# Kernel optimization log

Measured on AMD Instinct MI355X. Metric: run time of the kernel, lower is better.

Reference implementation:

```python
import jax, jax.numpy as jnp
import numpy as np

N_NODES = 50000
N_EDGES = 800000
F_IN = 128
UNIQUE_USER = 64
HIDDEN = 64
HEADS = 4


def _glorot(key, shape):
    fan_in, fan_out = shape[0], shape[-1]
    lim = (6.0 / (fan_in + fan_out)) ** 0.5
    return jax.random.uniform(key, shape, jnp.float32, -lim, lim)


def setup_inputs() -> dict:
    key = jax.random.key(0)
    ks = jax.random.split(key, 16)
    x = jax.random.normal(ks[0], (N_NODES, F_IN), jnp.float32)
    edge_index = jax.random.randint(ks[1], (2, N_EDGES), 0, N_NODES, jnp.int64)
    return {
        "x": x,
        "edge_index": edge_index,
        # lazy Linear layers (PyG Linear: y = x @ W + b)
        "lin1_w": _glorot(ks[2], (F_IN, UNIQUE_USER)),
        "lin1_b": jnp.zeros((UNIQUE_USER,), jnp.float32),
        "lin2_w": _glorot(ks[3], (F_IN, HIDDEN)),
        "lin2_b": jnp.zeros((HIDDEN,), jnp.float32),
        "lin3_w": _glorot(ks[4], (HIDDEN, HIDDEN)),
        "lin3_b": jnp.zeros((HIDDEN,), jnp.float32),
        # FeaStConv 1: in=UNIQUE_USER, out=HIDDEN, heads=HEADS
        "conv1_w": _glorot(ks[5], (UNIQUE_USER, HEADS * HIDDEN)),
        "conv1_u": _glorot(ks[6], (UNIQUE_USER, HEADS)),
        "conv1_c": jnp.zeros((HEADS,), jnp.float32),
        "conv1_bias": jnp.zeros((HIDDEN,), jnp.float32),
        # FeaStConv 2: in=HIDDEN, out=HIDDEN, heads=HEADS
        "conv2_w": _glorot(ks[7], (HIDDEN, HEADS * HIDDEN)),
        "conv2_u": _glorot(ks[8], (HIDDEN, HEADS)),
        "conv2_c": jnp.zeros((HEADS,), jnp.float32),
        "conv2_bias": jnp.zeros((HIDDEN,), jnp.float32),
    }


def feast_conv(x, edge_index, w, u, c, bias):
    # PyG FeaStConv, add_self_loops=False, aggr='mean'
    src, dst = edge_index[0], edge_index[1]  # message flows src(j) -> dst(i)
    x_j = x[src]                              # [E, Fin] gather
    x_i = x[dst]                              # [E, Fin] gather
    heads = u.shape[1]
    out_ch = w.shape[1] // heads
    # attention over heads: q = softmax((x_j - x_i) @ u + c)
    q = jax.nn.softmax((x_j - x_i) @ u + c, axis=-1)          # [E, H]
    w3 = w.reshape(w.shape[0], heads, out_ch)                  # [Fin, H, D]
    # message_e = sum_h q[e,h] * (x_j[e] @ W_h)
    msg = jnp.einsum('ef,fhd,eh->ed', x_j, w3, q)              # [E, D]
    agg = jax.ops.segment_sum(msg, dst, num_segments=N_NODES)  # [N, D]
    cnt = jax.ops.segment_sum(jnp.ones((msg.shape[0],), msg.dtype), dst,
                              num_segments=N_NODES)
    out = agg / jnp.clip(cnt, 1.0)[:, None]
    return out + bias


def reference(x, edge_index, lin1_w, lin1_b, lin2_w, lin2_b, lin3_w, lin3_b,
              conv1_w, conv1_u, conv1_c, conv1_bias,
              conv2_w, conv2_u, conv2_c, conv2_bias):
    h = feast_conv(x @ lin1_w + lin1_b, edge_index,
                   conv1_w, conv1_u, conv1_c, conv1_bias) + (x @ lin2_w + lin2_b)
    h = jax.nn.relu(h)
    h = feast_conv(h, edge_index,
                   conv2_w, conv2_u, conv2_c, conv2_bias) + (h @ lin3_w + lin3_b)
    return jax.nn.relu(h)
```

## Files before the change

### kernel.cpp

```cpp
#include <hip/hip_runtime.h>

#define NN 50000
#define NE 800000
#define NBUCK ((NN + 255) / 256)
#define EPB 4096
#define BCAP 8192
#define QCAP 512

typedef unsigned int uint32;
typedef unsigned short ushort16;
typedef __attribute__((ext_vector_type(8))) short bf16x8;
typedef __attribute__((ext_vector_type(4))) float f32x4;

__device__ __forceinline__ ushort16 f2bf(float f) {
    uint32 u = __float_as_uint(f);
    u += 0x7fff + ((u >> 16) & 1);
    return (ushort16)(u >> 16);
}
__device__ __forceinline__ float bf_lo(uint32 u) {
    return __uint_as_float(u << 16);
}
__device__ __forceinline__ float bf_hi(uint32 u) {
    return __uint_as_float(u & 0xffff0000u);
}
__device__ __forceinline__ bf16x8 pack8(const float4 a, const float4 b) {
    union { bf16x8 v; ushort16 u[8]; } r;
    r.u[0] = f2bf(a.x); r.u[1] = f2bf(a.y); r.u[2] = f2bf(a.z); r.u[3] = f2bf(a.w);
    r.u[4] = f2bf(b.x); r.u[5] = f2bf(b.y); r.u[6] = f2bf(b.z); r.u[7] = f2bf(b.w);
    return r.v;
}
__device__ __forceinline__ float4 softq(const float4 ts, const float4 td,
                                        const float4 tc, const float invdeg) {
    const float l0 = ts.x - td.x + tc.x;
    const float l1 = ts.y - td.y + tc.y;
    const float l2 = ts.z - td.z + tc.z;
    const float l3 = ts.w - td.w + tc.w;
    const float mx = fmaxf(fmaxf(l0, l1), fmaxf(l2, l3));
    const float e0 = __expf(l0 - mx);
    const float e1 = __expf(l1 - mx);
    const float e2 = __expf(l2 - mx);
    const float e3 = __expf(l3 - mx);
    const float sden = invdeg / (e0 + e1 + e2 + e3);
    return make_float4(e0 * sden, e1 * sden, e2 * sden, e3 * sden);
}

__device__ __forceinline__ float multireduce16(const float* tl, int m) {
    float t8[8];
#pragma unroll
    for (int i = 0; i < 8; ++i) {
        const float a0 = tl[2 * i], b0 = tl[2 * i + 1];
        const float oa = __shfl_xor(a0, 1, 64), ob = __shfl_xor(b0, 1, 64);
        t8[i] = ((m & 1) == 0) ? (a0 + oa) : (b0 + ob);
    }
    float t4[4];
#pragma unroll
    for (int i = 0; i < 4; ++i) {
        const float a0 = t8[2 * i], b0 = t8[2 * i + 1];
        const float oa = __shfl_xor(a0, 2, 64), ob = __shfl_xor(b0, 2, 64);
        t4[i] = ((m & 2) == 0) ? (a0 + oa) : (b0 + ob);
    }
    float t2[2];
#pragma unroll
    for (int i = 0; i < 2; ++i) {
        const float a0 = t4[2 * i], b0 = t4[2 * i + 1];
        const float oa = __shfl_xor(a0, 4, 64), ob = __shfl_xor(b0, 4, 64);
        t2[i] = ((m & 4) == 0) ? (a0 + oa) : (b0 + ob);
    }
    const float a0 = t2[0], b0 = t2[1];
    const float oa = __shfl_xor(a0, 8, 64), ob = __shfl_xor(b0, 8, 64);
    return ((m & 8) == 0) ? (a0 + oa) : (b0 + ob);
}

__device__ __forceinline__ ushort16 packp_val(const float* __restrict__ w, int i) {
    const int j  = i & 7;
    const int ln = (i >> 3) & 63;
    const int s  = (i >> 9) & 7;
    const int cc = i >> 12;
    const int k  = s * 32 + ((ln >> 4) * 8) + j;
    const int n  = cc * 16 + (ln & 15);
    return f2bf(w[(k >> 2) * 256 + (k & 3) * 64 + n]);
}

__global__ __launch_bounds__(256) void k_packall(
    const float* __restrict__ w1, const float* __restrict__ w2,
    const float* __restrict__ wc1, const float* __restrict__ wc2,
    const float* __restrict__ wl3,
    ushort16* __restrict__ pw12, ushort16* __restrict__ pwc1,
    ushort16* __restrict__ pwc2, ushort16* __restrict__ pwl3,
    int* __restrict__ bcnt)
{
    const int gid = blockIdx.x * 256 + threadIdx.x;
    if (gid < 16384) {
        const int i = gid;
        const int j  = i & 7;
        const int ln = (i >> 3) & 63;
        const int s  = (i >> 9) & 3;
        const int cc = i >> 11;
        const int k  = s * 32 + ((ln >> 4) * 8) + j;
        const int n  = cc * 16 + (ln & 15);
        pw12[i] = f2bf((n < 64) ? w1[k * 64 + n] : w2[k * 64 + (n - 64)]);
    } else if (gid < 32768) {
        pwc1[gid - 16384] = packp_val(wc1, gid - 16384);
    } else if (gid < 49152) {
        pwc2[gid - 32768] = packp_val(wc2, gid - 32768);
    } else if (gid < 53248) {
        const int i = gid - 49152;
        const int j  = i & 7;
        const int ln = (i >> 3) & 63;
        const int s  = (i >> 9) & 1;
        const int cc = i >> 10;
        const int k  = s * 32 + ((ln >> 4) * 8) + j;
        const int n  = cc * 16 + (ln & 15);
        pwl3[i] = f2bf(wl3[k * 64 + n]);
    } else if (gid < 53504) {
        bcnt[gid - 53248] = 0;
    }
}

__global__ __launch_bounds__(256) void k_lin12(
    const float* __restrict__ x, const ushort16* __restrict__ pw,
    const float* __restrict__ b1, const float* __restrict__ b2,
    const float* __restrict__ u,
    ushort16* __restrict__ ab, float* __restrict__ skip,
    float* __restrict__ tOut)
{
    const int tid = threadIdx.x;
    const int lane = tid & 63;
    const int g = tid >> 6;
    const int m = lane & 15;
    const int quad = lane >> 4;
    const int rowBase = blockIdx.x * 64 + g * 16;

    const int arow = min(rowBase + m, NN - 1);
    const float* xr = x + (size_t)arow * 128 + quad * 8;

    f32x4 acc[8];
#pragma unroll
    for (int c = 0; c < 8; ++c)
#pragma unroll
        for (int r = 0; r < 4; ++r) acc[c][r] = 0.f;

#pragma unroll
    for (int s = 0; s < 4; ++s) {
        const float4 xa = *(const float4*)(xr + s * 32);
        const float4 xb = *(const float4*)(xr + s * 32 + 4);
        const bf16x8 af = pack8(xa, xb);
#pragma unroll
        for (int c = 0; c < 8; ++c) {
            const bf16x8 bf = *(const bf16x8*)&pw[((c * 4 + s) * 64 + lane) * 8];
            acc[c] = __builtin_amdgcn_mfma_f32_16x16x32_bf16(af, bf, acc[c], 0, 0, 0);
        }
    }

    float tl[16];
#pragma unroll
    for (int i = 0; i < 16; ++i) tl[i] = 0.f;

#pragma unroll
    for (int c = 0; c < 8; ++c) {
        const int colg = c * 16 + m;
        const float bv = (colg < 64) ? b1[colg] : b2[colg - 64];
#pragma unroll
        for (int reg = 0; reg < 4; ++reg) {
            const float v = acc[c][reg] + bv;
            const int gr = rowBase + quad * 4 + reg;
            if (gr < NN) {
                if (c < 4) ab[gr * 64 + colg] = f2bf(v);
                else       skip[gr * 64 + (colg - 64)] = v;
            }
            if (c < 4) {
                const float4 uv = ((const float4*)u)[colg];
                tl[reg * 4 + 0] += v * uv.x;
                tl[reg * 4 + 1] += v * uv.y;
                tl[reg * 4 + 2] += v * uv.z;
                tl[reg * 4 + 3] += v * uv.w;
            }
        }
    }

    const float tv = multireduce16(tl, m);
    const int gidx = rowBase * 4 + (quad << 4) + m;
    if (gidx < NN * 4) tOut[gidx] = tv;
}

__global__ __launch_bounds__(256) void k_lin3m(
    const ushort16* __restrict__ hb, const ushort16* __restrict__ pw,
    const float* __restrict__ b, float* __restrict__ outp)
{
    const int tid = threadIdx.x;
    const int lane = tid & 63;
    const int g = tid >> 6;
    const int m = lane & 15;
    const int quad = lane >> 4;
    const int rowBase = blockIdx.x * 64 + g * 16;

    const int arow = min(rowBase + m, NN - 1);
    const ushort16* zrow = hb + (size_t)arow * 64 + quad * 8;

    f32x4 acc[4];
#pragma unroll
    for (int c = 0; c < 4; ++c)
#pragma unroll
        for (int r = 0; r < 4; ++r) acc[c][r] = 0.f;

#pragma unroll
    for (int s = 0; s < 2; ++s) {
        const bf16x8 af = *(const bf16x8*)(zrow + s * 32);
#pragma unroll
        for (int c = 0; c < 4; ++c) {
            const bf16x8 bf = *(const bf16x8*)&pw[((c * 2 + s) * 64 + lane) * 8];
            acc[c] = __builtin_amdgcn_mfma_f32_16x16x32_bf16(af, bf, acc[c], 0, 0, 0);
        }
    }

#pragma unroll
    for (int c = 0; c < 4; ++c) {
        const int colg = c * 16 + m;
        const float bv = b[colg];
#pragma unroll
        for (int reg = 0; reg < 4; ++reg) {
            const int gr = rowBase + quad * 4 + reg;
            if (gr < NN) outp[gr * 64 + colg] = acc[c][reg] + bv;
        }
    }
}

__global__ __launch_bounds__(256) void k_bin(const int* __restrict__ ei,
                                             int* __restrict__ bcnt,
                                             uint32* __restrict__ pairs)
{
    __shared__ int hist[NBUCK];
    __shared__ int gbase[NBUCK];
    const int t = threadIdx.x;
    const int base = blockIdx.x * EPB;

    for (int b = t; b < NBUCK; b += 256) hist[b] = 0;
    __syncthreads();

    uint32 pk[16];
    int bk[16], rk[16];
#pragma unroll
    for (int k = 0; k < 16; ++k) {
        const int e = base + k * 256 + t;
        if (e < NE) {
            const int s = ei[e];
            const int d = ei[NE + e];
            bk[k] = d >> 8;
            pk[k] = (uint32)s | ((uint32)(d & 255) << 16);
            rk[k] = atomicAdd(&hist[bk[k]], 1);
        }
    }
    __syncthreads();

    for (int b = t; b < NBUCK; b += 256)
        gbase[b] = hist[b] ? atomicAdd(&bcnt[b], hist[b]) : 0;
    __syncthreads();

#pragma unroll
    for (int k = 0; k < 16; ++k) {
        const int e = base + k * 256 + t;
        if (e < NE) pairs[(size_t)bk[k] * BCAP + gbase[bk[k]] + rk[k]] = pk[k];
    }
}

__global__ __launch_bounds__(256) void k_binscat(const uint32* __restrict__ pairs,
                                                 const int* __restrict__ bcnt,
                                                 int* __restrict__ row_ptr,
                                                 int* __restrict__ ssrc)
{
    __shared__ int sb[256];
    __shared__ int hist[256];
    __shared__ int s[256];
    __shared__ int lptr[256];
    __shared__ int lcur[256];
    const int b = blockIdx.x;
    const int t = threadIdx.x;
    const int total = bcnt[b];
    const uint32* pb = pairs + (size_t)b * BCAP;

    sb[t] = (t < NBUCK) ? bcnt[t] : 0;
    __syncthreads();
    for (int off = 1; off < 256; off <<= 1) {
        const int v = (t >= off) ? sb[t - off] : 0;
        __syncthreads();
        sb[t] += v;
        __syncthreads();
    }
    const int base = sb[b] - total;
    if (b == 0 && t == 0) row_ptr[NN] = NE;

    hist[t] = 0;
    __syncthreads();
    for (int e = t; e < total; e += 256) atomicAdd(&hist[pb[e] >> 16], 1);
    __syncthreads();

    const int v = hist[t];
    s[t] = v;
    __syncthreads();
    for (int off = 1; off < 256; off <<= 1) {
        const int u = (t >= off) ? s[t - off] : 0;
        __syncthreads();
        s[t] += u;
        __syncthreads();
    }
    const int excl = base + s[t] - v;
    lptr[t] = excl;
    lcur[t] = 0;
    const int n = (b << 8) + t;
    if (n < NN) row_ptr[n] = excl;
    __syncthreads();

    for (int e = t; e < total; e += 256) {
        const uint32 p = pb[e];
        const int d = p >> 16;
        const int r = atomicAdd(&lcur[d], 1);
        ssrc[lptr[d] + r] = (int)(p & 0xffffu);
    }
}

__global__ __launch_bounds__(256) void k_aggpost(
    const int* __restrict__ row_ptr, const int* __restrict__ ssrc,
    const float* __restrict__ t, const uint32* __restrict__ abu,
    const float* __restrict__ c,
    const ushort16* __restrict__ pw, const float* __restrict__ bias,
    const float* __restrict__ skip,
    float* __restrict__ out, ushort16* __restrict__ outb,
    const float* __restrict__ uproj, float* __restrict__ tOut)
{
    __shared__ float4 ql[QCAP];
    __shared__ char zl[16 * 512];
    __shared__ float t_lds[4][64];
    __shared__ float4 tnode[16];
    __shared__ float invdegs[16];

    const int tid = threadIdx.x;
    const int lane = tid & 63;
    const int w = tid >> 6;
    const int half = lane >> 5;
    const int u = lane & 31;
    const int nodeBase = blockIdx.x * 16;

    const float4 tc = *(const float4*)c;

    int rr = 0;
    if (lane < 7) {
        const int off = (lane < 5) ? (w * 4 + lane) : ((lane == 5) ? 0 : 16);
        rr = row_ptr[nodeBase + off];
    }
    const int rp0 = __shfl(rr, 0, 64);
    const int rp1 = __shfl(rr, 1, 64);
    const int rp2 = __shfl(rr, 2, 64);
    const int rp3 = __shfl(rr, 3, 64);
    const int rp4 = __shfl(rr, 4, 64);
    const int r0b = __shfl(rr, 5, 64);
    const int r1b = __shfl(rr, 6, 64);

    if (lane < 4) {
        tnode[w * 4 + lane] = ((const float4*)t)[nodeBase + w * 4 + lane];
        const int a = (lane == 0) ? rp0 : (lane == 1) ? rp1 : (lane == 2) ? rp2 : rp3;
        const int b = (lane == 0) ? rp1 : (lane == 1) ? rp2 : (lane == 2) ? rp3 : rp4;
        invdegs[w * 4 + lane] = (b > a) ? 1.f / (float)(b - a) : 0.f;
    }

    const bool fit = (r1b - r0b) <= QCAP;

    if (fit) {
        for (int i = rp0 + lane; i < rp4; i += 64) {
            const int se = ssrc[i];
            const int dl = (i >= rp1) + (i >= rp2) + (i >= rp3);
            const float4 ts = ((const float4*)t)[se];
            const float4 q = softq(ts, tnode[w * 4 + dl], tc, invdegs[w * 4 + dl]);
            ql[i - r0b] = make_float4(q.y, q.z, q.w, __int_as_float(se));
        }
    }

#define ACCUM3(QA, AV)                                                 \
    {                                                                  \
        const float v0 = bf_lo(AV), v1 = bf_hi(AV);                    \
        const float q0 = invdeg - (QA).x - (QA).y - (QA).z;            \
        z00 += q0 * v0;     z01 += q0 * v1;                            \
        z10 += (QA).x * v0; z11 += (QA).x * v1;                        \
        z20 += (QA).y * v0; z21 += (QA).y * v1;                        \
        z30 += (QA).z * v0; z31 += (QA).z * v1;                        \
    }
#define ACCUM4(Q4, AV)                                                 \
    {                                                                  \
        const float v0 = bf_lo(AV), v1 = bf_hi(AV);                    \
        z00 += (Q4).x * v0; z01 += (Q4).x * v1;                        \
        z10 += (Q4).y * v0; z11 += (Q4).y * v1;                        \
        z20 += (Q4).z * v0; z21 += (Q4).z * v1;                        \
        z30 += (Q4).w * v0; z31 += (Q4).w * v1;                        \
    }

#pragma unroll
    for (int nn = 0; nn < 4; ++nn) {
        const int nloc = w * 4 + nn;
        const int r0 = (nn == 0) ? rp0 : (nn == 1) ? rp1 : (nn == 2) ? rp2 : rp3;
        const int r1 = (nn == 0) ? rp1 : (nn == 1) ? rp2 : (nn == 2) ? rp3 : rp4;
        const float invdeg = (r1 > r0) ? 1.f / (float)(r1 - r0) : 0.f;

        float z00 = 0.f, z01 = 0.f, z10 = 0.f, z11 = 0.f;
        float z20 = 0.f, z21 = 0.f, z30 = 0.f, z31 = 0.f;

        if (fit) {
            const float4* qb = ql - r0b;
            int idx = r0;
            for (; idx + 7 < r1; idx += 8) {
                const float4 qa0 = qb[idx + half];
                const float4 qa1 = qb[idx + 2 + half];
                const float4 qa2 = qb[idx + 4 + half];
                const float4 qa3 = qb[idx + 6 + half];
                const uint32 av0 = abu[__float_as_int(qa0.w) * 32 + u];
                const uint32 av1 = abu[__float_as_int(qa1.w) * 32 + u];
                const uint32 av2 = abu[__float_as_int(qa2.w) * 32 + u];
                const uint32 av3 = abu[__float_as_int(qa3.w) * 32 + u];
                ACCUM3(qa0, av0) ACCUM3(qa1, av1)
                ACCUM3(qa2, av2) ACCUM3(qa3, av3)
            }
            for (; idx + 1 < r1; idx += 2) {
                const float4 qa = qb[idx + half];
                const uint32 av = abu[__float_as_int(qa.w) * 32 + u];
                ACCUM3(qa, av)
            }
            if (idx < r1 && half == 0) {
                const float4 qa = qb[idx];
                const uint32 av = abu[__float_as_int(qa.w) * 32 + u];
                ACCUM3(qa, av)
            }
        } else {
            const float4 td = tnode[nloc];
            int idx = r0;
            for (; idx + 1 < r1; idx += 2) {
                const int se = ssrc[idx + half];
                const uint32 av = abu[se * 32 + u];
                const float4 q4 = softq(((const float4*)t)[se], td, tc, invdeg);
                ACCUM4(q4, av)
            }
            if (idx < r1 && half == 0) {
                const int se = ssrc[idx];
                const uint32 av = abu[se * 32 + u];
                const float4 q4 = softq(((const float4*)t)[se], td, tc, invdeg);
                ACCUM4(q4, av)
            }
        }
#undef ACCUM3
#undef ACCUM4

        z00 += __shfl_xor(z00, 32, 64); z01 += __shfl_xor(z01, 32, 64);
        z10 += __shfl_xor(z10, 32, 64); z11 += __shfl_xor(z11, 32, 64);
        z20 += __shfl_xor(z20, 32, 64); z21 += __shfl_xor(z21, 32, 64);
        z30 += __shfl_xor(z30, 32, 64); z31 += __shfl_xor(z31, 32, 64);

        if (half == 0) {
            uint4 pk;
            pk.x = (uint32)f2bf(z00) | ((uint32)f2bf(z10) << 16);
            pk.y = (uint32)f2bf(z20) | ((uint32)f2bf(z30) << 16);
            pk.z = (uint32)f2bf(z01) | ((uint32)f2bf(z11) << 16);
            pk.w = (uint32)f2bf(z21) | ((uint32)f2bf(z31) << 16);
            *(uint4*)(zl + nloc * 512 + ((u * 16) ^ ((nloc & 7) << 4))) = pk;
        }
    }
    __syncthreads();

    const int m = lane & 15;
    const int quad = lane >> 4;

    f32x4 acc;
#pragma unroll
    for (int r = 0; r < 4; ++r) acc[r] = 0.f;

#pragma unroll
    for (int s = 0; s < 8; ++s) {
        const bf16x8 af = *(const bf16x8*)(zl + m * 512 +
                            ((s * 64 + quad * 16) ^ ((m & 7) << 4)));
        const bf16x8 bf = *(const bf16x8*)&pw[((w * 8 + s) * 64 + lane) * 8];
        acc = __builtin_amdgcn_mfma_f32_16x16x32_bf16(af, bf, acc, 0, 0, 0);
    }

    const int colg = w * 16 + m;
    const float bv = bias[colg];

    float tl[16];
#pragma unroll
    for (int i = 0; i < 16; ++i) tl[i] = 0.f;

#pragma unroll
    for (int reg = 0; reg < 4; ++reg) {
        const int gr = nodeBase + quad * 4 + reg;
        const float v = fmaxf(acc[reg] + bv + skip[gr * 64 + colg], 0.f);
        if (out)  out[gr * 64 + colg]  = v;
        if (outb) outb[gr * 64 + colg] = f2bf(v);
        if (tOut) {
            const float4 uv = ((const float4*)uproj)[colg];
            tl[reg * 4 + 0] += v * uv.x;
            tl[reg * 4 + 1] += v * uv.y;
            tl[reg * 4 + 2] += v * uv.z;
            tl[reg * 4 + 3] += v * uv.w;
        }
    }

    if (tOut) {
        const float tv = multireduce16(tl, m);
        t_lds[w][lane] = tv;
        __syncthreads();
        if (w == 0) {
            const float tvf = t_lds[0][lane] + t_lds[1][lane] +
                              t_lds[2][lane] + t_lds[3][lane];
            tOut[nodeBase * 4 + lane] = tvf;
        }
    }
}

extern "C" void kernel_launch(void* const* d_in, const int* in_sizes, int n_in,
                              void* d_out, int out_size, void* d_ws, size_t ws_size,
                              hipStream_t stream) {
    const float* x       = (const float*)d_in[0];
    const int*   ei      = (const int*)d_in[1];
    const float* lin1_w  = (const float*)d_in[2];
    const float* lin1_b  = (const float*)d_in[3];
    const float* lin2_w  = (const float*)d_in[4];
    const float* lin2_b  = (const float*)d_in[5];
    const float* lin3_w  = (const float*)d_in[6];
    const float* lin3_b  = (const float*)d_in[7];
    const float* conv1_w = (const float*)d_in[8];
    const float* conv1_u = (const float*)d_in[9];
    const float* conv1_c = (const float*)d_in[10];
    const float* conv1_bias = (const float*)d_in[11];
    const float* conv2_w = (const float*)d_in[12];
    const float* conv2_u = (const float*)d_in[13];
    const float* conv2_c = (const float*)d_in[14];
    const float* conv2_bias = (const float*)d_in[15];
    float* out = (float*)d_out;

    char* p = (char*)d_ws;
    float* skip   = (float*)p;           p += (size_t)NN * 64 * 4;
    float* tt     = (float*)p;           p += (size_t)NN * 4 * 4;
    float* tt2    = (float*)p;           p += (size_t)NN * 4 * 4;
    ushort16* ab  = (ushort16*)p;        p += (size_t)NN * 64 * 2;
    ushort16* hb  = (ushort16*)p;        p += (size_t)NN * 64 * 2;
    ushort16* pw12 = (ushort16*)p;       p += 16384 * 2;
    ushort16* pwc1 = (ushort16*)p;       p += 16384 * 2;
    ushort16* pwc2 = (ushort16*)p;       p += 16384 * 2;
    ushort16* pwl3 = (ushort16*)p;       p += 4096 * 2;
    int* ssrc     = (int*)p;             p += (size_t)NE * 4;
    int* row_ptr  = (int*)p;             p += (size_t)(NN + 1) * 4;
    int* bcnt     = (int*)p;             p += 256 * 4;
    uint32* pairs = (uint32*)p;          p += (size_t)NBUCK * BCAP * 4;

    k_packall<<<209, 256, 0, stream>>>(lin1_w, lin2_w, conv1_w, conv2_w, lin3_w,
                                       pw12, pwc1, pwc2, pwl3, bcnt);
    k_bin<<<(NE + EPB - 1) / EPB, 256, 0, stream>>>(ei, bcnt, pairs);
    k_binscat<<<NBUCK, 256, 0, stream>>>(pairs, bcnt, row_ptr, ssrc);

    k_lin12<<<(NN + 63) / 64, 256, 0, stream>>>(x, pw12, lin1_b, lin2_b, conv1_u,
                                                ab, skip, tt);
    k_aggpost<<<NN / 16, 256, 0, stream>>>(row_ptr, ssrc, tt,
                                           (const uint32*)ab, conv1_c,
                                           pwc1, conv1_bias, skip,
                                           nullptr, hb, conv2_u, tt2);

    k_lin3m<<<(NN + 63) / 64, 256, 0, stream>>>(hb, pwl3, lin3_b, skip);
    k_aggpost<<<NN / 16, 256, 0, stream>>>(row_ptr, ssrc, tt2,
                                           (const uint32*)hb, conv2_c,
                                           pwc2, conv2_bias, skip,
                                           out, nullptr, nullptr, nullptr);
}
```

Baseline: 224.3 us.

## Fuse lin3 GEMM into first aggpost and widen gather to 8-byte loads

Removes the separate k_lin3m launch by computing the lin3 projection inside the first aggregation kernel. The post-ReLU bf16 tile is staged in a swizzled LDS buffer and fed to MFMA, and the result overwrites skip in place. The gather loop is also reorganized so each lane loads 8 bytes (4 bf16 features) and handles quarter-wave edges, with 16 accumulators and a two-step shuffle reduction. This saves a kernel launch and a reread of hb, at the cost of more registers, an extra LDS buffer, and an in-place skip overwrite that relies on each block reading only its own rows.

Measured after the change: 218.6 us. 2.5% less time.

```diff
diff --git a/kernel.cpp b/kernel.cpp
--- a/kernel.cpp
+++ b/kernel.cpp
@@ -183,48 +183,6 @@
     if (gidx < NN * 4) tOut[gidx] = tv;
 }
 
-__global__ __launch_bounds__(256) void k_lin3m(
-    const ushort16* __restrict__ hb, const ushort16* __restrict__ pw,
-    const float* __restrict__ b, float* __restrict__ outp)
-{
-    const int tid = threadIdx.x;
-    const int lane = tid & 63;
-    const int g = tid >> 6;
-    const int m = lane & 15;
-    const int quad = lane >> 4;
-    const int rowBase = blockIdx.x * 64 + g * 16;
-
-    const int arow = min(rowBase + m, NN - 1);
-    const ushort16* zrow = hb + (size_t)arow * 64 + quad * 8;
-
-    f32x4 acc[4];
-#pragma unroll
-    for (int c = 0; c < 4; ++c)
-#pragma unroll
-        for (int r = 0; r < 4; ++r) acc[c][r] = 0.f;
-
-#pragma unroll
-    for (int s = 0; s < 2; ++s) {
-        const bf16x8 af = *(const bf16x8*)(zrow + s * 32);
-#pragma unroll
-        for (int c = 0; c < 4; ++c) {
-            const bf16x8 bf = *(const bf16x8*)&pw[((c * 2 + s) * 64 + lane) * 8];
-            acc[c] = __builtin_amdgcn_mfma_f32_16x16x32_bf16(af, bf, acc[c], 0, 0, 0);
-        }
-    }
-
-#pragma unroll
-    for (int c = 0; c < 4; ++c) {
-        const int colg = c * 16 + m;
-        const float bv = b[colg];
-#pragma unroll
-        for (int reg = 0; reg < 4; ++reg) {
-            const int gr = rowBase + quad * 4 + reg;
-            if (gr < NN) outp[gr * 64 + colg] = acc[c][reg] + bv;
-        }
-    }
-}
-
 __global__ __launch_bounds__(256) void k_bin(const int* __restrict__ ei,
                                              int* __restrict__ bcnt,
                                              uint32* __restrict__ pairs)
@@ -323,12 +281,14 @@
     const float* __restrict__ t, const uint32* __restrict__ abu,
     const float* __restrict__ c,
     const ushort16* __restrict__ pw, const float* __restrict__ bias,
-    const float* __restrict__ skip,
+    float* skip,
     float* __restrict__ out, ushort16* __restrict__ outb,
-    const float* __restrict__ uproj, float* __restrict__ tOut)
+    const float* __restrict__ uproj, float* __restrict__ tOut,
+    const ushort16* __restrict__ pwl3, const float* __restrict__ b3)
 {
     __shared__ float4 ql[QCAP];
     __shared__ char zl[16 * 512];
+    __shared__ char hl[16 * 128];
     __shared__ float t_lds[4][64];
     __shared__ float4 tnode[16];
     __shared__ float invdegs[16];
@@ -336,11 +296,12 @@
     const int tid = threadIdx.x;
     const int lane = tid & 63;
     const int w = tid >> 6;
-    const int half = lane >> 5;
-    const int u = lane & 31;
+    const int qtr = lane >> 4;
+    const int u4 = lane & 15;
     const int nodeBase = blockIdx.x * 16;
 
     const float4 tc = *(const float4*)c;
+    const uint2* ab8 = (const uint2*)abu;
 
     int rr = 0;
     if (lane < 7) {
@@ -374,22 +335,25 @@
         }
     }
 
-#define ACCUM3(QA, AV)                                                 \
+#define ACCQ(QA, AV)                                                   \
     {                                                                  \
-        const float v0 = bf_lo(AV), v1 = bf_hi(AV);                    \
-        const float q0 = invdeg - (QA).x - (QA).y - (QA).z;            \
-        z00 += q0 * v0;     z01 += q0 * v1;                            \
-        z10 += (QA).x * v0; z11 += (QA).x * v1;                        \
-        z20 += (QA).y * v0; z21 += (QA).y * v1;                        \
-        z30 += (QA).z * v0; z31 += (QA).z * v1;                        \
-    }
-#define ACCUM4(Q4, AV)                                                 \
+        const float q1 = (QA).x, q2 = (QA).y, q3 = (QA).z;             \
+        const float q0 = invdeg - q1 - q2 - q3;                        \
+        const float v0 = bf_lo((AV).x), v1 = bf_hi((AV).x);            \
+        const float v2 = bf_lo((AV).y), v3 = bf_hi((AV).y);            \
+        z[0] += q0 * v0;  z[1] += q0 * v1;  z[2] += q0 * v2;  z[3] += q0 * v3;  \
+        z[4] += q1 * v0;  z[5] += q1 * v1;  z[6] += q1 * v2;  z[7] += q1 * v3;  \
+        z[8] += q2 * v0;  z[9] += q2 * v1;  z[10] += q2 * v2; z[11] += q2 * v3; \
+        z[12] += q3 * v0; z[13] += q3 * v1; z[14] += q3 * v2; z[15] += q3 * v3; \
+    }
+#define ACCQ4(Q4, AV)                                                  \
     {                                                                  \
-        const float v0 = bf_lo(AV), v1 = bf_hi(AV);                    \
-        z00 += (Q4).x * v0; z01 += (Q4).x * v1;                        \
-        z10 += (Q4).y * v0; z11 += (Q4).y * v1;                        \
-        z20 += (Q4).z * v0; z21 += (Q4).z * v1;                        \
-        z30 += (Q4).w * v0; z31 += (Q4).w * v1;                        \
+        const float v0 = bf_lo((AV).x), v1 = bf_hi((AV).x);            \
+        const float v2 = bf_lo((AV).y), v3 = bf_hi((AV).y);            \
+        z[0] += (Q4).x * v0;  z[1] += (Q4).x * v1;  z[2] += (Q4).x * v2;  z[3] += (Q4).x * v3;  \
+        z[4] += (Q4).y * v0;  z[5] += (Q4).y * v1;  z[6] += (Q4).y * v2;  z[7] += (Q4).y * v3;  \
+        z[8] += (Q4).z * v0;  z[9] += (Q4).z * v1;  z[10] += (Q4).z * v2; z[11] += (Q4).z * v3; \
+        z[12] += (Q4).w * v0; z[13] += (Q4).w * v1; z[14] += (Q4).w * v2; z[15] += (Q4).w * v3; \
     }
 
 #pragma unroll
@@ -399,65 +363,65 @@
         const int r1 = (nn == 0) ? rp1 : (nn == 1) ? rp2 : (nn == 2) ? rp3 : rp4;
         const float invdeg = (r1 > r0) ? 1.f / (float)(r1 - r0) : 0.f;
 
-        float z00 = 0.f, z01 = 0.f, z10 = 0.f, z11 = 0.f;
-        float z20 = 0.f, z21 = 0.f, z30 = 0.f, z31 = 0.f;
+        float z[16];
+#pragma unroll
+        for (int i = 0; i < 16; ++i) z[i] = 0.f;
 
         if (fit) {
             const float4* qb = ql - r0b;
             int idx = r0;
             for (; idx + 7 < r1; idx += 8) {
-                const float4 qa0 = qb[idx + half];
-                const float4 qa1 = qb[idx + 2 + half];
-                const float4 qa2 = qb[idx + 4 + half];
-                const float4 qa3 = qb[idx + 6 + half];
-                const uint32 av0 = abu[__float_as_int(qa0.w) * 32 + u];
-                const uint32 av1 = abu[__float_as_int(qa1.w) * 32 + u];
-                const uint32 av2 = abu[__float_as_int(qa2.w) * 32 + u];
-                const uint32 av3 = abu[__float_as_int(qa3.w) * 32 + u];
-                ACCUM3(qa0, av0) ACCUM3(qa1, av1)
-                ACCUM3(qa2, av2) ACCUM3(qa3, av3)
+                const float4 qa0 = qb[idx + qtr];
+                const float4 qa1 = qb[idx + 4 + qtr];
+                const uint2 av0 = ab8[__float_as_int(qa0.w) * 16 + u4];
+                const uint2 av1 = ab8[__float_as_int(qa1.w) * 16 + u4];
+                ACCQ(qa0, av0) ACCQ(qa1, av1)
             }
-            for (; idx + 1 < r1; idx += 2) {
-                const float4 qa = qb[idx + half];
-                const uint32 av = abu[__float_as_int(qa.w) * 32 + u];
-                ACCUM3(qa, av)
+            if (idx + qtr < r1) {
+                const float4 qa = qb[idx + qtr];
+                const uint2 av = ab8[__float_as_int(qa.w) * 16 + u4];
+                ACCQ(qa, av)
             }
-            if (idx < r1 && half == 0) {
-                const float4 qa = qb[idx];
-                const uint32 av = abu[__float_as_int(qa.w) * 32 + u];
-                ACCUM3(qa, av)
+            if (idx + 4 + qtr < r1) {
+                const float4 qa = qb[idx + 4 + qtr];
+                const uint2 av = ab8[__float_as_int(qa.w) * 16 + u4];
+                ACCQ(qa, av)
             }
         } else {
             const float4 td = tnode[nloc];
-            int idx = r0;
-            for (; idx + 1 < r1; idx += 2) {
-                const int se = ssrc[idx + half];
-                const uint32 av = abu[se * 32 + u];
-                const float4 q4 = softq(((const float4*)t)[se], td, tc, invdeg);
-                ACCUM4(q4, av)
+            for (int idx = r0; idx < r1; idx += 4) {
+                const int e = idx + qtr;
+                if (e < r1) {
+                    const int se = ssrc[e];
+                    const uint2 av = ab8[se * 16 + u4];
+                    const float4 q4 = softq(((const float4*)t)[se], td, tc, invdeg);
+                    ACCQ4(q4, av)
+                }
             }
-            if (idx < r1 && half == 0) {
-                const int se = ssrc[idx];
-                const uint32 av = abu[se * 32 + u];
-                const float4 q4 = softq(((const float4*)t)[se], td, tc, invdeg);
-                ACCUM4(q4, av)
-            }
-        }
-#undef ACCUM3
-#undef ACCUM4
-
-        z00 += __shfl_xor(z00, 32, 64); z01 += __shfl_xor(z01, 32, 64);
-        z10 += __shfl_xor(z10, 32, 64); z11 += __shfl_xor(z11, 32, 64);
-        z20 += __shfl_xor(z20, 32, 64); z21 += __shfl_xor(z21, 32, 64);
-        z30 += __shfl_xor(z30, 32, 64); z31 += __shfl_xor(z31, 32, 64);
-
-        if (half == 0) {
+        }
+#undef ACCQ
+#undef ACCQ4
+
+#pragma unroll
+        for (int i = 0; i < 16; ++i) {
+            z[i] += __shfl_xor(z[i], 16, 64);
+            z[i] += __shfl_xor(z[i], 32, 64);
+        }
+
+        if (qtr == 0) {
             uint4 pk;
-            pk.x = (uint32)f2bf(z00) | ((uint32)f2bf(z10) << 16);
-            pk.y = (uint32)f2bf(z20) | ((uint32)f2bf(z30) << 16);
-            pk.z = (uint32)f2bf(z01) | ((uint32)f2bf(z11) << 16);
-            pk.w = (uint32)f2bf(z21) | ((uint32)f2bf(z31) << 16);
-            *(uint4*)(zl + nloc * 512 + ((u * 16) ^ ((nloc & 7) << 4))) = pk;
+            pk.x = (uint32)f2bf(z[0])  | ((uint32)f2bf(z[4])  << 16);
+            pk.y = (uint32)f2bf(z[8])  | ((uint32)f2bf(z[12]) << 16);
+            pk.z = (uint32)f2bf(z[1])  | ((uint32)f2bf(z[5])  << 16);
+            pk.w = (uint32)f2bf(z[9])  | ((uint32)f2bf(z[13]) << 16);
+            *(uint4*)(zl + nloc * 512 + (((2 * u4) * 16) ^ ((nloc & 7) << 4))) = pk;
+        } else if (qtr == 1) {
+            uint4 pk;
+            pk.x = (uint32)f2bf(z[2])  | ((uint32)f2bf(z[6])  << 16);
+            pk.y = (uint32)f2bf(z[10]) | ((uint32)f2bf(z[14]) << 16);
+            pk.z = (uint32)f2bf(z[3])  | ((uint32)f2bf(z[7])  << 16);
+            pk.w = (uint32)f2bf(z[11]) | ((uint32)f2bf(z[15]) << 16);
+            *(uint4*)(zl + nloc * 512 + (((2 * u4 + 1) * 16) ^ ((nloc & 7) << 4))) = pk;
         }
     }
     __syncthreads();
@@ -490,6 +454,10 @@
         const float v = fmaxf(acc[reg] + bv + skip[gr * 64 + colg], 0.f);
         if (out)  out[gr * 64 + colg]  = v;
         if (outb) outb[gr * 64 + colg] = f2bf(v);
+        if (pwl3) {
+            const int row = quad * 4 + reg;
+            *(ushort16*)(hl + ((row * 128 + colg * 2) ^ ((row & 7) << 4))) = f2bf(v);
+        }
         if (tOut) {
             const float4 uv = ((const float4*)uproj)[colg];
             tl[reg * 4 + 0] += v * uv.x;
@@ -502,11 +470,31 @@
     if (tOut) {
         const float tv = multireduce16(tl, m);
         t_lds[w][lane] = tv;
-        __syncthreads();
-        if (w == 0) {
-            const float tvf = t_lds[0][lane] + t_lds[1][lane] +
-                              t_lds[2][lane] + t_lds[3][lane];
-            tOut[nodeBase * 4 + lane] = tvf;
+    }
+    __syncthreads();
+
+    if (tOut && w == 0) {
+        const float tvf = t_lds[0][lane] + t_lds[1][lane] +
+                          t_lds[2][lane] + t_lds[3][lane];
+        tOut[nodeBase * 4 + lane] = tvf;
+    }
+
+    if (pwl3) {
+        f32x4 acc3;
+#pragma unroll
+        for (int r = 0; r < 4; ++r) acc3[r] = 0.f;
+#pragma unroll
+        for (int s = 0; s < 2; ++s) {
+            const bf16x8 af = *(const bf16x8*)(hl +
+                                ((m * 128 + quad * 16 + s * 64) ^ ((m & 7) << 4)));
+            const bf16x8 bf = *(const bf16x8*)&pwl3[((w * 2 + s) * 64 + lane) * 8];
+            acc3 = __builtin_amdgcn_mfma_f32_16x16x32_bf16(af, bf, acc3, 0, 0, 0);
+        }
+        const float b3v = b3[colg];
+#pragma unroll
+        for (int reg = 0; reg < 4; ++reg) {
+            const int gr = nodeBase + quad * 4 + reg;
+            skip[gr * 64 + colg] = acc3[reg] + b3v;
         }
     }
 }
@@ -557,11 +545,12 @@
     k_aggpost<<<NN / 16, 256, 0, stream>>>(row_ptr, ssrc, tt,
                                            (const uint32*)ab, conv1_c,
                                            pwc1, conv1_bias, skip,
-                                           nullptr, hb, conv2_u, tt2);
-
-    k_lin3m<<<(NN + 63) / 64, 256, 0, stream>>>(hb, pwl3, lin3_b, skip);
+                                           nullptr, hb, conv2_u, tt2,
+                                           pwl3, lin3_b);
+
     k_aggpost<<<NN / 16, 256, 0, stream>>>(row_ptr, ssrc, tt2,
                                            (const uint32*)hb, conv2_c,
                                            pwc2, conv2_bias, skip,
-                                           out, nullptr, nullptr, nullptr);
-}
+                                           out, nullptr, nullptr, nullptr,
+                                           nullptr, nullptr);
+}
```

## Fuse lin3 GEMM into first aggregation epilogue and unroll gather loop by 16

Applied to the files above, without the earlier changes.

The separate lin3 kernel is removed. The first k_aggpost now stages the bf16 relu output in a swizzled LDS tile and runs a 16x64x64 MFMA against the lin3 weights, writing the result over the skip buffer in place. This saves one kernel launch and a reread of hb from global memory, at the cost of extra LDS and a block-wide sync that now runs even when tOut is null. The edge gather loop also gains a 16-edge unrolled stage to put more independent loads in flight, which adds register pressure.

After: 225.5 us. About the same (+0.5%).

```diff
diff --git a/kernel.cpp b/kernel.cpp
--- a/kernel.cpp
+++ b/kernel.cpp
@@ -183,48 +183,6 @@
     if (gidx < NN * 4) tOut[gidx] = tv;
 }
 
-__global__ __launch_bounds__(256) void k_lin3m(
-    const ushort16* __restrict__ hb, const ushort16* __restrict__ pw,
-    const float* __restrict__ b, float* __restrict__ outp)
-{
-    const int tid = threadIdx.x;
-    const int lane = tid & 63;
-    const int g = tid >> 6;
-    const int m = lane & 15;
-    const int quad = lane >> 4;
-    const int rowBase = blockIdx.x * 64 + g * 16;
-
-    const int arow = min(rowBase + m, NN - 1);
-    const ushort16* zrow = hb + (size_t)arow * 64 + quad * 8;
-
-    f32x4 acc[4];
-#pragma unroll
-    for (int c = 0; c < 4; ++c)
-#pragma unroll
-        for (int r = 0; r < 4; ++r) acc[c][r] = 0.f;
-
-#pragma unroll
-    for (int s = 0; s < 2; ++s) {
-        const bf16x8 af = *(const bf16x8*)(zrow + s * 32);
-#pragma unroll
-        for (int c = 0; c < 4; ++c) {
-            const bf16x8 bf = *(const bf16x8*)&pw[((c * 2 + s) * 64 + lane) * 8];
-            acc[c] = __builtin_amdgcn_mfma_f32_16x16x32_bf16(af, bf, acc[c], 0, 0, 0);
-        }
-    }
-
-#pragma unroll
-    for (int c = 0; c < 4; ++c) {
-        const int colg = c * 16 + m;
-        const float bv = b[colg];
-#pragma unroll
-        for (int reg = 0; reg < 4; ++reg) {
-            const int gr = rowBase + quad * 4 + reg;
-            if (gr < NN) outp[gr * 64 + colg] = acc[c][reg] + bv;
-        }
-    }
-}
-
 __global__ __launch_bounds__(256) void k_bin(const int* __restrict__ ei,
                                              int* __restrict__ bcnt,
                                              uint32* __restrict__ pairs)
@@ -323,12 +281,14 @@
     const float* __restrict__ t, const uint32* __restrict__ abu,
     const float* __restrict__ c,
     const ushort16* __restrict__ pw, const float* __restrict__ bias,
-    const float* __restrict__ skip,
+    float* skip,
     float* __restrict__ out, ushort16* __restrict__ outb,
-    const float* __restrict__ uproj, float* __restrict__ tOut)
+    const float* __restrict__ uproj, float* __restrict__ tOut,
+    const ushort16* __restrict__ pwl3, const float* __restrict__ b3)
 {
     __shared__ float4 ql[QCAP];
     __shared__ char zl[16 * 512];
+    __shared__ char hl[16 * 128];
     __shared__ float t_lds[4][64];
     __shared__ float4 tnode[16];
     __shared__ float invdegs[16];
@@ -405,6 +365,28 @@
         if (fit) {
             const float4* qb = ql - r0b;
             int idx = r0;
+            for (; idx + 15 < r1; idx += 16) {
+                const float4 qa0 = qb[idx + half];
+                const float4 qa1 = qb[idx + 2 + half];
+                const float4 qa2 = qb[idx + 4 + half];
+                const float4 qa3 = qb[idx + 6 + half];
+                const float4 qa4 = qb[idx + 8 + half];
+                const float4 qa5 = qb[idx + 10 + half];
+                const float4 qa6 = qb[idx + 12 + half];
+                const float4 qa7 = qb[idx + 14 + half];
+                const uint32 av0 = abu[__float_as_int(qa0.w) * 32 + u];
+                const uint32 av1 = abu[__float_as_int(qa1.w) * 32 + u];
+                const uint32 av2 = abu[__float_as_int(qa2.w) * 32 + u];
+                const uint32 av3 = abu[__float_as_int(qa3.w) * 32 + u];
+                const uint32 av4 = abu[__float_as_int(qa4.w) * 32 + u];
+                const uint32 av5 = abu[__float_as_int(qa5.w) * 32 + u];
+                const uint32 av6 = abu[__float_as_int(qa6.w) * 32 + u];
+                const uint32 av7 = abu[__float_as_int(qa7.w) * 32 + u];
+                ACCUM3(qa0, av0) ACCUM3(qa1, av1)
+                ACCUM3(qa2, av2) ACCUM3(qa3, av3)
+                ACCUM3(qa4, av4) ACCUM3(qa5, av5)
+                ACCUM3(qa6, av6) ACCUM3(qa7, av7)
+            }
             for (; idx + 7 < r1; idx += 8) {
                 const float4 qa0 = qb[idx + half];
                 const float4 qa1 = qb[idx + 2 + half];
@@ -490,6 +472,10 @@
         const float v = fmaxf(acc[reg] + bv + skip[gr * 64 + colg], 0.f);
         if (out)  out[gr * 64 + colg]  = v;
         if (outb) outb[gr * 64 + colg] = f2bf(v);
+        if (pwl3) {
+            const int row = quad * 4 + reg;
+            *(ushort16*)(hl + ((row * 128 + colg * 2) ^ ((row & 7) << 4))) = f2bf(v);
+        }
         if (tOut) {
             const float4 uv = ((const float4*)uproj)[colg];
             tl[reg * 4 + 0] += v * uv.x;
@@ -502,11 +488,31 @@
     if (tOut) {
         const float tv = multireduce16(tl, m);
         t_lds[w][lane] = tv;
-        __syncthreads();
-        if (w == 0) {
-            const float tvf = t_lds[0][lane] + t_lds[1][lane] +
-                              t_lds[2][lane] + t_lds[3][lane];
-            tOut[nodeBase * 4 + lane] = tvf;
+    }
+    __syncthreads();
+
+    if (tOut && w == 0) {
+        const float tvf = t_lds[0][lane] + t_lds[1][lane] +
+                          t_lds[2][lane] + t_lds[3][lane];
+        tOut[nodeBase * 4 + lane] = tvf;
+    }
+
+    if (pwl3) {
+        f32x4 acc3;
+#pragma unroll
+        for (int r = 0; r < 4; ++r) acc3[r] = 0.f;
+#pragma unroll
+        for (int s = 0; s < 2; ++s) {
+            const bf16x8 af = *(const bf16x8*)(hl +
+                                ((m * 128 + quad * 16 + s * 64) ^ ((m & 7) << 4)));
+            const bf16x8 bf = *(const bf16x8*)&pwl3[((w * 2 + s) * 64 + lane) * 8];
+            acc3 = __builtin_amdgcn_mfma_f32_16x16x32_bf16(af, bf, acc3, 0, 0, 0);
+        }
+        const float b3v = b3[colg];
+#pragma unroll
+        for (int reg = 0; reg < 4; ++reg) {
+            const int gr = nodeBase + quad * 4 + reg;
+            skip[gr * 64 + colg] = acc3[reg] + b3v;
         }
     }
 }
@@ -557,11 +563,12 @@
     k_aggpost<<<NN / 16, 256, 0, stream>>>(row_ptr, ssrc, tt,
                                            (const uint32*)ab, conv1_c,
                                            pwc1, conv1_bias, skip,
-                                           nullptr, hb, conv2_u, tt2);
-
-    k_lin3m<<<(NN + 63) / 64, 256, 0, stream>>>(hb, pwl3, lin3_b, skip);
+                                           nullptr, hb, conv2_u, tt2,
+                                           pwl3, lin3_b);
+
     k_aggpost<<<NN / 16, 256, 0, stream>>>(row_ptr, ssrc, tt2,
                                            (const uint32*)hb, conv2_c,
                                            pwc2, conv2_bias, skip,
-                                           out, nullptr, nullptr, nullptr);
-}
+                                           out, nullptr, nullptr, nullptr,
+                                           nullptr, nullptr);
+}
```
